# Performance work log

Hardware: AMD Instinct MI355X
Metric: run time of the kernel (lower is better)

The kernel has to match this reference:

```python
import jax, jax.numpy as jnp
import numpy as np

ALPHA = 2000.0   # alpha (bandwidth penalty)
K = 8            # number of modes
MAX_N = 20       # max ADMM iterations; tol=0 -> loop always runs MAX_N-1 iters
DC = False


def setup_inputs() -> dict:
    key = jax.random.key(0)
    signal = jax.random.normal(key, (16, 8192), dtype=jnp.float32)  # (C, T)
    return {"signal": signal}


def _forward(signal):
    C, T = signal.shape
    F = 2 * T
    # mirror extension -> (C, 2T)
    f = jnp.concatenate([signal[:, :T // 2][:, ::-1], signal, signal[:, T // 2:][:, ::-1]], axis=1)
    t = jnp.linspace(1.0 / F, 1.0, F)
    freqs = (t - 0.5 - 1.0 / F).astype(jnp.float32)                  # (F,)
    # NOTE: torch.fft.fftshift with default dim shifts ALL dims (incl. channel dim);
    # jnp.fft.fftshift with axes=None matches this behavior exactly.
    f_hat = jnp.fft.fftshift(jnp.fft.fft(f))
    f_hat_plus = f_hat.at[:, :F // 2].set(0)                         # zero negative freqs
    fpos = f_hat_plus.T.astype(jnp.complex64)                        # (F, C)
    freqs_c = freqs.astype(jnp.complex64)
    fh = freqs[F // 2:]                                              # positive freqs (F/2,)
    alpha_c = jnp.complex64(ALPHA)

    omega0 = ((0.5 / K) * jnp.arange(K, dtype=jnp.float32)).astype(jnp.complex64)  # init == 1
    u0 = jnp.zeros((F, K, C), jnp.complex64)
    sum0 = jnp.zeros((F, C), jnp.complex64)

    def omega_update(u_k):                                           # u_k: (F, C)
        p = jnp.abs(u_k[F // 2:, :]) ** 2                            # (F/2, C)
        return (jnp.sum(fh @ p) / jnp.sum(p)).astype(jnp.complex64)

    def step(carry, _):
        u_prev, omega_prev, sum_uk = carry
        sum_uk = sum_uk + u_prev[:, K - 1, :] - u_prev[:, 0, :]
        us, omegas = [], []
        for k in range(K):                                           # sequential mode recurrence
            if k > 0:
                sum_uk = sum_uk + us[k - 1] - u_prev[:, k, :]
            # torch uses omega from the PREVIOUS outer iteration for all modes
            denom = 1.0 + alpha_c * jnp.square(freqs_c - omega_prev[k])   # (F,)
            u_k = (fpos - sum_uk) / denom[:, None]   # lamda_hat stays 0 (never updated in torch)
            us.append(u_k)
            if k == 0 and DC:
                omegas.append(jnp.complex64(0.0))
            else:
                omegas.append(omega_update(u_k))
        u_curr = jnp.stack(us, axis=1)                               # (F, K, C)
        omega_curr = jnp.stack(omegas)                               # (K,)
        return (u_curr, omega_curr, sum_uk), omega_curr

    (u_fin, _, _), omega_hist = jax.lax.scan(step, (u0, omega0, sum0), None, length=MAX_N - 1)
    omega = jnp.concatenate([omega0[None, :], omega_hist], axis=0)   # (MAX_N, K)

    # Hermitian completion of the half-spectrum (matches torch index assignments & order)
    pos = u_fin[F // 2:, :, :]                                       # (F/2, K, C)
    u_hat = jnp.zeros((F, K, C), jnp.complex64)
    u_hat = u_hat.at[F // 2:].set(pos)
    u_hat = u_hat.at[jnp.arange(F // 2, 0, -1)].set(jnp.conj(pos))   # overwrites bin F/2 w/ conj
    u_hat = u_hat.at[0].set(jnp.conj(u_hat[-1]))

    u_time = jnp.fft.ifft(jnp.fft.ifftshift(u_hat, axes=0), axis=0).real  # (F, K, C)
    u_c = jnp.transpose(u_time, (1, 0, 2)).astype(jnp.complex64)          # (K, F, C)
    u_c = u_c[:, F // 4:3 * F // 4, :]                                    # crop mirror -> (K, T, C)
    u_hat2 = jnp.conj(jnp.fft.fftshift(jnp.fft.fft(u_c, axis=1), axes=1)) # (K, T, C)
    u_hat2 = jnp.transpose(u_hat2, (1, 0, 2))                             # (T, K, C)
    # torch applies ifftshift with dim=-1, which is the CHANNEL dim here; replicate faithfully
    u_out = jnp.fft.ifftshift(u_c, axes=-1).real                          # (K, T, C)
    return u_out, u_hat2, omega


def reference(signal):
    return _forward(signal)
```

## Files before the change

kernel.cpp:

```cpp
#include <hip/hip_runtime.h>
#include <math.h>

#define NPAIR 131072
#define STEPS 19
#define VMD_BLOCKS 256
#define ND_BANKS 16

#define SW(a) ((a) ^ (((a) >> 5) & 31))

#define LD_RLX(p)    __hip_atomic_load((p),       __ATOMIC_RELAXED, __HIP_MEMORY_SCOPE_AGENT)
#define ST_RLX(p,v)  __hip_atomic_store((p),(v),  __ATOMIC_RELAXED, __HIP_MEMORY_SCOPE_AGENT)
#define FAA_RLX(p,v) __hip_atomic_fetch_add((p),(v),__ATOMIC_RELAXED, __HIP_MEMORY_SCOPE_AGENT)

#define D_NDB   0
#define D_CNT   4864
#define D_OHIST 5400

__device__ __forceinline__ float2 cadd(float2 a, float2 b){ return make_float2(a.x+b.x, a.y+b.y); }
__device__ __forceinline__ float2 csub(float2 a, float2 b){ return make_float2(a.x-b.x, a.y-b.y); }
__device__ __forceinline__ float2 cmul(float2 a, float2 b){
    return make_float2(a.x*b.x - a.y*b.y, a.x*b.y + a.y*b.x);
}
template<int SGN>
__device__ __forceinline__ float2 imul(float2 a){
    return (SGN > 0) ? make_float2(-a.y, a.x) : make_float2(a.y, -a.x);
}

template<int SGN>
__device__ __forceinline__ void dft8(const float2* a, float2* y){
    const float C = 0.70710678118654752f;
    const float sg = (SGN > 0) ? 1.f : -1.f;
    float2 t0 = cadd(a[0], a[4]), t1 = csub(a[0], a[4]);
    float2 t2 = cadd(a[2], a[6]), t3 = imul<SGN>(csub(a[2], a[6]));
    float2 E0 = cadd(t0, t2), E2 = csub(t0, t2), E1 = cadd(t1, t3), E3 = csub(t1, t3);
    float2 s0 = cadd(a[1], a[5]), s1 = csub(a[1], a[5]);
    float2 s2 = cadd(a[3], a[7]), s3 = imul<SGN>(csub(a[3], a[7]));
    float2 O0 = cadd(s0, s2), O2 = csub(s0, s2), O1 = cadd(s1, s3), O3 = csub(s1, s3);
    float2 w1 = make_float2(C, sg * C), w3 = make_float2(-C, sg * C);
    float2 R0 = O0, R1 = cmul(O1, w1), R2 = imul<SGN>(O2), R3 = cmul(O3, w3);
    y[0] = cadd(E0, R0); y[4] = csub(E0, R0);
    y[1] = cadd(E1, R1); y[5] = csub(E1, R1);
    y[2] = cadd(E2, R2); y[6] = csub(E2, R2);
    y[3] = cadd(E3, R3); y[7] = csub(E3, R3);
}

template<int SGN>
__device__ void lds_fft8192_r8(float2* lds, int tid){
    #pragma unroll
    for (int pi = 0; pi < 4; pi++){
        int ls = 3 * pi;
        int s  = 1 << ls;
        int nn = 8192 >> ls;
        int q = tid & (s - 1);
        float2 a[8], y[8];
        #pragma unroll
        for (int r = 0; r < 8; r++) a[r] = lds[SW(tid + (r << 10))];
        __syncthreads();
        dft8<SGN>(a, y);
        int p = tid >> ls;
        float ang = (float)(2 * p) / (float)nn;
        float sn, cs;
        sincospif(SGN > 0 ? ang : -ang, &sn, &cs);
        float2 w = make_float2(cs, sn);
        float2 wk = make_float2(1.f, 0.f);
        int o = q + ((tid - q) << 3);
        lds[SW(o)] = y[0];
        #pragma unroll
        for (int k = 1; k < 8; k++){
            wk = cmul(wk, w);
            lds[SW(o + (k << ls))] = cmul(y[k], wk);
        }
        __syncthreads();
    }
    #pragma unroll
    for (int w4 = 0; w4 < 4; w4++){
        int idx = (w4 << 10) + tid;
        float2 a = lds[SW(idx)], b = lds[SW(idx + 4096)];
        lds[SW(idx)]        = cadd(a, b);
        lds[SW(idx + 4096)] = csub(a, b);
    }
    __syncthreads();
}

template<int SGN>
__device__ void lds_fft4096_r8(float2* lds, int tid){
    #pragma unroll
    for (int pi = 0; pi < 4; pi++){
        int ls = 3 * pi;
        int s  = 1 << ls;
        int nn = 4096 >> ls;
        float2 a[8], y[8];
        int q = tid & (s - 1);
        if (tid < 512){
            #pragma unroll
            for (int r = 0; r < 8; r++) a[r] = lds[SW(tid + (r << 9))];
        }
        __syncthreads();
        if (tid < 512){
            dft8<SGN>(a, y);
            int p = tid >> ls;
            float ang = (float)(2 * p) / (float)nn;
            float sn, cs;
            sincospif(SGN > 0 ? ang : -ang, &sn, &cs);
            float2 w = make_float2(cs, sn);
            float2 wk = make_float2(1.f, 0.f);
            int o = q + ((tid - q) << 3);
            lds[SW(o)] = y[0];
            #pragma unroll
            for (int k = 1; k < 8; k++){
                wk = cmul(wk, w);
                lds[SW(o + (k << ls))] = cmul(y[k], wk);
            }
        }
        __syncthreads();
    }
}

__device__ __forceinline__ void gbar(int* CNT, int grp, int round){
    int target = 16 * round;
    int old = FAA_RLX(&CNT[grp * 32], 1);
    bool released = false;
    if (old == target - 1){
        int rold = FAA_RLX(&CNT[512], 1);
        if (rold == target - 1){
            #pragma unroll
            for (int g = 0; g < 16; g++)
                ST_RLX(&CNT[576 + g * 32], round);
            released = true;
        }
    }
    if (!released)
        while (LD_RLX(&CNT[576 + grp * 32]) < round)
            __builtin_amdgcn_s_sleep(1);
}

__global__ __launch_bounds__(512, 2) void k_vmd_all(const float* __restrict__ sig,
                                                    float2* __restrict__ C,
                                                    float2* __restrict__ U,
                                                    double* __restrict__ D){
    extern __shared__ float2 lds[];
    double* NDB   = D + D_NDB;
    int*    CNT   = (int*)(D + D_CNT);
    double* OHIST = D + D_OHIST;

    int tid = blockIdx.x * 512 + threadIdx.x;
    int lane = threadIdx.x & 63, wv = threadIdx.x >> 6;
    int mybank = (blockIdx.x & (ND_BANKS - 1)) * 16;
    int grp = blockIdx.x >> 4;

    if (blockIdx.x < 64){
        int bb = blockIdx.x;
        int cwa = bb >> 2, r4 = bb & 3;
        int cs = (cwa + 8) & 15;
        const float* sp = sig + cs * 8192;
        #pragma unroll
        for (int i = 0; i < 8; i++){
            int p = i * 512 + threadIdx.x;
            int x = 4 * p + r4;
            int mx = (x < 4096) ? (4095 - x) : ((x < 12288) ? (x - 4096) : (20479 - x));
            lds[SW(p)] = make_float2(sp[mx], 0.f);
        }
        __syncthreads();
        lds_fft4096_r8<-1>(lds, threadIdx.x);
        float2* dst = C + (size_t)bb * 4096;
        #pragma unroll
        for (int i = 0; i < 8; i++){
            int j2 = i * 512 + threadIdx.x;
            ST_RLX(&dst[j2], lds[SW(j2)]);
        }
    }
    __syncthreads();
    if (threadIdx.x == 0) gbar(CNT, grp, 1);
    __syncthreads();

    int j = tid & 8191;
    int cw = tid >> 13;
    float fr = (float)j / 16384.0f;
    const float2* Cb = C + (size_t)(cw * 4) * 4096;
    int m = j & 4095;
    float2 C0 = LD_RLX(&Cb[m]),        C1 = LD_RLX(&Cb[4096 + m]);
    float2 C2 = LD_RLX(&Cb[8192 + m]), C3 = LD_RLX(&Cb[12288 + m]);
    float s1, c1, s2, c2;
    sincospif(-(float)j / 8192.0f, &s1, &c1);
    sincospif(-(float)j / 4096.0f, &s2, &c2);
    float2 w1 = make_float2(c1, s1), w2 = make_float2(c2, s2), w3 = cmul(w1, w2);
    float2 fv = cadd(cadd(C0, cmul(w1, C1)), cadd(cmul(w2, C2), cmul(w3, C3)));
    float fx = fv.x, fy = fv.y;
    float urx[8], ury[8], om[8];
    #pragma unroll
    for (int k = 0; k < 8; k++){ urx[k] = 0.f; ury[k] = 0.f; om[k] = 0.0625f * (float)k; }
    __shared__ float  lred[8][16];
    __shared__ double ndls[256];
    __shared__ double om_s[8];

    for (int step = 0; step < STEPS; step++){
        if (step > 0){
            #pragma unroll
            for (int k = 0; k < 8; k++) om[k] = (float)om_s[k];
        }
        float sx = 0.f, sy = 0.f;
        #pragma unroll
        for (int k = 1; k < 8; k++){ sx += urx[k]; sy += ury[k]; }
        float lx = 0.f, ly = 0.f, nloc[8], dloc[8];
        #pragma unroll
        for (int k = 0; k < 8; k++){
            if (k > 0){ sx += lx - urx[k]; sy += ly - ury[k]; }
            float d = fr - om[k];
            float den = 1.0f + 2000.0f * d * d;
            float rden = 1.0f / den;
            float nx = (fx - sx) * rden, ny = (fy - sy) * rden;
            urx[k] = nx; ury[k] = ny;
            lx = nx; ly = ny;
            float pw = nx * nx + ny * ny;
            nloc[k] = fr * pw; dloc[k] = pw;
        }
        float s8[8];
        {
            bool hi = (lane & 32) != 0;
            #pragma unroll
            for (int k = 0; k < 8; k++){
                float t = hi ? nloc[k] : dloc[k];
                float r = __shfl_xor(t, 32);
                s8[k] = (hi ? dloc[k] : nloc[k]) + r;
            }
        }
        float s4v[4];
        {
            bool hi = (lane & 16) != 0;
            #pragma unroll
            for (int k = 0; k < 4; k++){
                float t = hi ? s8[k] : s8[k + 4];
                float r = __shfl_xor(t, 16);
                s4v[k] = (hi ? s8[k + 4] : s8[k]) + r;
            }
        }
        float s2v[2];
        {
            bool hi = (lane & 8) != 0;
            #pragma unroll
            for (int k = 0; k < 2; k++){
                float t = hi ? s4v[k] : s4v[k + 2];
                float r = __shfl_xor(t, 8);
                s2v[k] = (hi ? s4v[k + 2] : s4v[k]) + r;
            }
        }
        float sv;
        {
            bool hi = (lane & 4) != 0;
            float t = hi ? s2v[0] : s2v[1];
            float r = __shfl_xor(t, 4);
            sv = (hi ? s2v[1] : s2v[0]) + r;
        }
        sv += __shfl_xor(sv, 2);
        sv += __shfl_xor(sv, 1);
        if ((lane & 3) == 0) lred[wv][lane >> 2] = sv;
        __syncthreads();
        if (threadIdx.x < 16){
            double sum = 0.0;
            #pragma unroll
            for (int w = 0; w < 8; w++) sum += (double)lred[w][threadIdx.x];
            atomicAdd(&NDB[step * 256 + mybank + threadIdx.x], sum);
        }
        __syncthreads();
        if (step < STEPS - 1){
            if (threadIdx.x == 0) gbar(CNT, grp, step + 2);
            __syncthreads();
            if (threadIdx.x < 256)
                ndls[threadIdx.x] = LD_RLX(&NDB[step * 256 + threadIdx.x]);
            __syncthreads();
            if (threadIdx.x < 8){
                double n_ = 0.0, d_ = 0.0;
                #pragma unroll
                for (int bk = 0; bk < ND_BANKS; bk++){
                    n_ += ndls[bk * 16 + threadIdx.x];
                    d_ += ndls[bk * 16 + 8 + threadIdx.x];
                }
                double v = n_ / d_;
                om_s[threadIdx.x] = v;
                if (blockIdx.x == 0)
                    ST_RLX(&OHIST[step * 8 + threadIdx.x], v);
            }
            __syncthreads();
        }
    }
    #pragma unroll
    for (int k = 0; k < 8; k++) U[k * NPAIR + tid] = make_float2(urx[k], ury[k]);
}

__global__ __launch_bounds__(1024) void k_stageCD(float2* __restrict__ U){
    extern __shared__ float2 lds[];
    int tid = threadIdx.x;
    int b = blockIdx.x;
    const float2* pos = U + b * 8192;
    float* slice = (float*)(U) + (size_t)b * 16384;
    const float inv = 1.0f / 16384.0f;
    #pragma unroll
    for (int r = 0; r < 8; r++){
        int p = r * 1024 + tid;
        float2 Hk, HkM;
        if (p == 0){
            Hk  = make_float2(pos[0].x, 0.f);
            HkM = make_float2(pos[8191].x, 0.f);
        } else {
            Hk = pos[p];
            float2 q2 = pos[8192 - p];
            HkM = make_float2(q2.x, -q2.y);
        }
        float2 S  = cadd(Hk, HkM);
        float2 Dv = csub(Hk, HkM);
        float sn, cn;
        sincospif((float)p / 8192.0f, &sn, &cn);
        float2 c = cmul(make_float2(cn, sn), Dv);
        lds[SW(p)] = make_float2(S.x - c.y, S.y + c.x);
    }
    __syncthreads();
    lds_fft8192_r8<1>(lds, tid);
    float2 zreg[4];
    #pragma unroll
    for (int q = 2; q < 6; q++){
        int n = q * 1024 + tid;
        float2 z = lds[SW(n)];
        zreg[q - 2] = make_float2(z.x * inv, z.y * inv);
        *(float2*)&slice[2 * n - 4096] = zreg[q - 2];
    }
    __syncthreads();
    #pragma unroll
    for (int q = 0; q < 4; q++)
        lds[SW(q * 1024 + tid)] = zreg[q];
    __syncthreads();
    lds_fft4096_r8<-1>(lds, tid);
    #pragma unroll
    for (int q = 0; q < 4; q++){
        int k = q * 1024 + tid;
        float2 Wk = lds[SW(k)];
        float2 Wm = lds[SW((4096 - k) & 4095)];
        float ax = 0.5f * (Wk.x + Wm.x);
        float dx = Wk.x - Wm.x, dy = Wk.y + Wm.y;
        float bx = 0.5f * dy, by = -0.5f * dx;
        float sn, cn;
        sincospif(-(float)k / 4096.0f, &sn, &cn);
        float rey = ax + cn * bx - sn * by;
        slice[12288 + k] = rey;
        if (k > 0) slice[12288 - k] = rey;
        else       slice[8192]      = Wk.x - Wk.y;
    }
}

__global__ __launch_bounds__(256) void k_outs(const float* __restrict__ U32,
                                              const double* __restrict__ Dbase,
                                              float* __restrict__ out){
    __shared__ double smemd[128 * 65 / 2 + 140];
    float* smem = (float*)smemd;
    int bx = blockIdx.x;
    int tid = threadIdx.x;
    if (bx < 256){
        float (*tile)[257] = (float(*)[257])smem;
        int k  = bx >> 5;
        int t0 = (bx & 31) * 256;
        #pragma unroll
        for (int cw = 0; cw < 16; cw++)
            tile[cw][tid] = U32[((size_t)(k * 16 + cw)) * 16384 + t0 + tid];
        __syncthreads();
        #pragma unroll
        for (int i = 0; i < 16; i++){
            int flat = i * 256 + tid;
            int dt = flat >> 4, ch = flat & 15;
            int cw = (ch + 8) & 15;
            out[(size_t)k * 131072 + t0 * 16 + flat] = tile[cw][dt];
        }
    } else if (bx < 384){
        float (*tile)[65] = (float(*)[65])smem;
        int t0 = (bx - 256) * 64;
        #pragma unroll
        for (int i = 0; i < 32; i++){
            int flat = i * 256 + tid;
            int b = flat >> 6, dt = flat & 63;
            tile[b][dt] = U32[(size_t)b * 16384 + 8192 + t0 + dt];
        }
        __syncthreads();
        #pragma unroll
        for (int i = 0; i < 32; i++){
            int flat = i * 256 + tid;
            int dt = flat >> 7, b = flat & 127;
            out[1048576 + (size_t)(t0 + dt) * 128 + b] = tile[b][dt];
        }
    } else {
        const double* NDB   = Dbase + D_NDB;
        const double* OHIST = Dbase + D_OHIST;
        double* dsm = smemd;
        if (tid < 256) dsm[tid] = NDB[18 * 256 + tid];
        __syncthreads();
        if (tid < 8){
            double n_ = 0.0, d_ = 0.0;
            #pragma unroll
            for (int bk = 0; bk < ND_BANKS; bk++){
                n_ += dsm[bk * 16 + tid];
                d_ += dsm[bk * 16 + 8 + tid];
            }
            dsm[256 + tid] = n_ / d_;
        }
        __syncthreads();
        if (tid < 160){
            int row = tid >> 3, k = tid & 7;
            double v;
            if (row == 0)       v = 0.0625 * (double)k;
            else if (row <= 18) v = OHIST[(row - 1) * 8 + k];
            else                v = dsm[256 + k];
            out[2097152 + tid] = (float)v;
        }
    }
}

extern "C" void kernel_launch(void* const* d_in, const int* in_sizes, int n_in,
                              void* d_out, int out_size, void* d_ws, size_t ws_size,
                              hipStream_t stream){
    const float* sig = (const float*)d_in[0];
    float* out = (float*)d_out;
    char* p = (char*)d_ws;
    float2* U = (float2*)p;
    float2* C = (float2*)p;
    double* D = (double*)(p + (size_t)8 * 1024 * 1024);

    hipMemsetAsync(D, 0, 5400 * sizeof(double), stream);
    k_vmd_all<<<dim3(VMD_BLOCKS), dim3(512), 32768, stream>>>(sig, C, U, D);
    k_stageCD<<<dim3(128), dim3(1024), 65536, stream>>>(U);
    k_outs<<<dim3(385), dim3(256), 0, stream>>>((const float*)U, D, out);
}
```

Before: 153.0 us.

## Fuse stageCD and output kernels via grid barrier; use plain stores with fences

Merges the spectral reconstruction kernel and the output transpose kernel into one launch, with a software grid barrier across the 128 blocks so the output phase reads completed slices. The generalized barrier takes a group count and uses a second counter region, zeroed by the enlarged memset. The relaxed atomic stores and loads of the FFT results in the main kernel become plain accesses guarded by thread fences. This removes one kernel launch and its gap, in exchange for a spin barrier and fewer, larger blocks doing the transpose work.

```diff
diff --git a/kernel.cpp b/kernel.cpp
--- a/kernel.cpp
+++ b/kernel.cpp
@@ -15,6 +15,8 @@
 #define D_NDB   0
 #define D_CNT   4864
 #define D_OHIST 5400
+#define D_CNT2  5544
+#define D_ZERO  5952
 
 __device__ __forceinline__ float2 cadd(float2 a, float2 b){ return make_float2(a.x+b.x, a.y+b.y); }
 __device__ __forceinline__ float2 csub(float2 a, float2 b){ return make_float2(a.x-b.x, a.y-b.y); }
@@ -116,21 +118,19 @@
     }
 }
 
-__device__ __forceinline__ void gbar(int* CNT, int grp, int round){
-    int target = 16 * round;
-    int old = FAA_RLX(&CNT[grp * 32], 1);
+__device__ __forceinline__ void gbar(int* cnt, int grp, int round, int ngroups){
+    int old = FAA_RLX(&cnt[grp * 32], 1);
     bool released = false;
-    if (old == target - 1){
-        int rold = FAA_RLX(&CNT[512], 1);
-        if (rold == target - 1){
-            #pragma unroll
-            for (int g = 0; g < 16; g++)
-                ST_RLX(&CNT[576 + g * 32], round);
+    if (old == 16 * round - 1){
+        int rold = FAA_RLX(&cnt[512], 1);
+        if (rold == ngroups * round - 1){
+            for (int g = 0; g < ngroups; g++)
+                ST_RLX(&cnt[576 + g * 32], round);
             released = true;
         }
     }
     if (!released)
-        while (LD_RLX(&CNT[576 + grp * 32]) < round)
+        while (LD_RLX(&cnt[576 + grp * 32]) < round)
             __builtin_amdgcn_s_sleep(1);
 }
 
@@ -166,11 +166,15 @@
         #pragma unroll
         for (int i = 0; i < 8; i++){
             int j2 = i * 512 + threadIdx.x;
-            ST_RLX(&dst[j2], lds[SW(j2)]);
-        }
-    }
-    __syncthreads();
-    if (threadIdx.x == 0) gbar(CNT, grp, 1);
+            dst[j2] = lds[SW(j2)];
+        }
+        __syncthreads();
+        __threadfence();
+    }
+    __syncthreads();
+    if (threadIdx.x == 0) gbar(CNT, grp, 1, 16);
+    __syncthreads();
+    __threadfence();
     __syncthreads();
 
     int j = tid & 8191;
@@ -178,8 +182,7 @@
     float fr = (float)j / 16384.0f;
     const float2* Cb = C + (size_t)(cw * 4) * 4096;
     int m = j & 4095;
-    float2 C0 = LD_RLX(&Cb[m]),        C1 = LD_RLX(&Cb[4096 + m]);
-    float2 C2 = LD_RLX(&Cb[8192 + m]), C3 = LD_RLX(&Cb[12288 + m]);
+    float2 C0 = Cb[m], C1 = Cb[4096 + m], C2 = Cb[8192 + m], C3 = Cb[12288 + m];
     float s1, c1, s2, c2;
     sincospif(-(float)j / 8192.0f, &s1, &c1);
     sincospif(-(float)j / 4096.0f, &s2, &c2);
@@ -263,7 +266,7 @@
         }
         __syncthreads();
         if (step < STEPS - 1){
-            if (threadIdx.x == 0) gbar(CNT, grp, step + 2);
+            if (threadIdx.x == 0) gbar(CNT, grp, step + 2, 16);
             __syncthreads();
             if (threadIdx.x < 256)
                 ndls[threadIdx.x] = LD_RLX(&NDB[step * 256 + threadIdx.x]);
@@ -287,12 +290,17 @@
     for (int k = 0; k < 8; k++) U[k * NPAIR + tid] = make_float2(urx[k], ury[k]);
 }
 
-__global__ __launch_bounds__(1024) void k_stageCD(float2* __restrict__ U){
+__global__ __launch_bounds__(1024) void k_cd_outs(float2* __restrict__ U,
+                                                  double* __restrict__ Dbase,
+                                                  float* __restrict__ out){
     extern __shared__ float2 lds[];
     int tid = threadIdx.x;
-    int b = blockIdx.x;
-    const float2* pos = U + b * 8192;
-    float* slice = (float*)(U) + (size_t)b * 16384;
+    int bx = blockIdx.x;
+    int*    CNT2  = (int*)(Dbase + D_CNT2);
+    const double* NDB   = Dbase + D_NDB;
+    const double* OHIST = Dbase + D_OHIST;
+    const float2* pos = U + bx * 8192;
+    float* slice = (float*)(U) + (size_t)bx * 16384;
     const float inv = 1.0f / 16384.0f;
     #pragma unroll
     for (int r = 0; r < 8; r++){
@@ -336,68 +344,75 @@
         float2 Wm = lds[SW((4096 - k) & 4095)];
         float ax = 0.5f * (Wk.x + Wm.x);
         float dx = Wk.x - Wm.x, dy = Wk.y + Wm.y;
-        float bx = 0.5f * dy, by = -0.5f * dx;
+        float bx2 = 0.5f * dy, by = -0.5f * dx;
         float sn, cn;
         sincospif(-(float)k / 4096.0f, &sn, &cn);
-        float rey = ax + cn * bx - sn * by;
+        float rey = ax + cn * bx2 - sn * by;
         slice[12288 + k] = rey;
         if (k > 0) slice[12288 - k] = rey;
         else       slice[8192]      = Wk.x - Wk.y;
     }
-}
-
-__global__ __launch_bounds__(256) void k_outs(const float* __restrict__ U32,
-                                              const double* __restrict__ Dbase,
-                                              float* __restrict__ out){
-    __shared__ double smemd[128 * 65 / 2 + 140];
-    float* smem = (float*)smemd;
-    int bx = blockIdx.x;
-    int tid = threadIdx.x;
-    if (bx < 256){
-        float (*tile)[257] = (float(*)[257])smem;
-        int k  = bx >> 5;
-        int t0 = (bx & 31) * 256;
-        #pragma unroll
-        for (int cw = 0; cw < 16; cw++)
-            tile[cw][tid] = U32[((size_t)(k * 16 + cw)) * 16384 + t0 + tid];
-        __syncthreads();
-        #pragma unroll
-        for (int i = 0; i < 16; i++){
-            int flat = i * 256 + tid;
-            int dt = flat >> 4, ch = flat & 15;
+    __syncthreads();
+    __threadfence();
+    __syncthreads();
+    if (tid == 0) gbar(CNT2, bx >> 4, 1, 8);
+    __syncthreads();
+    __threadfence();
+    __syncthreads();
+
+    const float* U32 = (const float*)U;
+    float* fl = (float*)lds;
+    float (*tile0)[257] = (float(*)[257])fl;
+    #pragma unroll
+    for (int ti2 = 0; ti2 < 2; ti2++){
+        int ti = 2 * bx + ti2;
+        int k  = ti >> 5;
+        int t0 = (ti & 31) * 256;
+        #pragma unroll
+        for (int i = 0; i < 4; i++){
+            int idx = i * 1024 + tid;
+            int cw = idx >> 8, dt = idx & 255;
+            tile0[cw][dt] = U32[((size_t)(k * 16 + cw)) * 16384 + t0 + dt];
+        }
+        __syncthreads();
+        #pragma unroll
+        for (int i = 0; i < 4; i++){
+            int f = i * 1024 + tid;
+            int dt = f >> 4, ch = f & 15;
             int cw = (ch + 8) & 15;
-            out[(size_t)k * 131072 + t0 * 16 + flat] = tile[cw][dt];
-        }
-    } else if (bx < 384){
-        float (*tile)[65] = (float(*)[65])smem;
-        int t0 = (bx - 256) * 64;
-        #pragma unroll
-        for (int i = 0; i < 32; i++){
-            int flat = i * 256 + tid;
-            int b = flat >> 6, dt = flat & 63;
-            tile[b][dt] = U32[(size_t)b * 16384 + 8192 + t0 + dt];
-        }
-        __syncthreads();
-        #pragma unroll
-        for (int i = 0; i < 32; i++){
-            int flat = i * 256 + tid;
-            int dt = flat >> 7, b = flat & 127;
-            out[1048576 + (size_t)(t0 + dt) * 128 + b] = tile[b][dt];
-        }
-    } else {
-        const double* NDB   = Dbase + D_NDB;
-        const double* OHIST = Dbase + D_OHIST;
-        double* dsm = smemd;
-        if (tid < 256) dsm[tid] = NDB[18 * 256 + tid];
+            out[(size_t)k * 131072 + t0 * 16 + f] = tile0[cw][dt];
+        }
+        __syncthreads();
+    }
+    {
+        float (*tile1)[65] = (float(*)[65])fl;
+        int t0 = bx * 64;
+        #pragma unroll
+        for (int i = 0; i < 8; i++){
+            int idx = i * 1024 + tid;
+            int b = idx >> 6, dt = idx & 63;
+            tile1[b][dt] = U32[(size_t)b * 16384 + 8192 + t0 + dt];
+        }
+        __syncthreads();
+        #pragma unroll
+        for (int i = 0; i < 8; i++){
+            int f = i * 1024 + tid;
+            int dt = f >> 7, b = f & 127;
+            out[1048576 + (size_t)(t0 + dt) * 128 + b] = tile1[b][dt];
+        }
+    }
+    if (bx == 0){
+        double* omsm = (double*)((char*)lds + 40960);
+        if (tid < 256) omsm[tid] = NDB[18 * 256 + tid];
         __syncthreads();
         if (tid < 8){
             double n_ = 0.0, d_ = 0.0;
             #pragma unroll
             for (int bk = 0; bk < ND_BANKS; bk++){
-                n_ += dsm[bk * 16 + tid];
-                d_ += dsm[bk * 16 + 8 + tid];
-            }
-            dsm[256 + tid] = n_ / d_;
+                n_ += omsm[bk * 16 + tid];
+                d_ += omsm[bk * 16 + 8 + tid];
+            }
+            omsm[256 + tid] = n_ / d_;
         }
         __syncthreads();
         if (tid < 160){
@@ -405,7 +420,7 @@
             double v;
             if (row == 0)       v = 0.0625 * (double)k;
             else if (row <= 18) v = OHIST[(row - 1) * 8 + k];
-            else                v = dsm[256 + k];
+            else                v = omsm[256 + k];
             out[2097152 + tid] = (float)v;
         }
     }
@@ -421,8 +436,7 @@
     float2* C = (float2*)p;
     double* D = (double*)(p + (size_t)8 * 1024 * 1024);
 
-    hipMemsetAsync(D, 0, 5400 * sizeof(double), stream);
+    hipMemsetAsync(D, 0, D_ZERO * sizeof(double), stream);
     k_vmd_all<<<dim3(VMD_BLOCKS), dim3(512), 32768, stream>>>(sig, C, U, D);
-    k_stageCD<<<dim3(128), dim3(1024), 65536, stream>>>(U);
-    k_outs<<<dim3(385), dim3(256), 0, stream>>>((const float*)U, D, out);
-}
+    k_cd_outs<<<dim3(128), dim3(1024), 65536, stream>>>(U, D, out);
+}
```

Measured after the change: 252.0 us. +64.7%, slower.
